# Kernel optimization log

Measured on AMD Instinct MI355X. Metric: run time of the kernel, lower is better.

The kernel has to match this reference:

```python
import jax, jax.numpy as jnp
import numpy as np
import math

KERNEL_SIZES = [3, 5, 7, 7, 9, 9]
DILATIONS = [1, 2, 1, 3, 1, 2]
NUM_HEADS = 6
HEAD_DIM = 32  # in_channels 192 / 6 heads


def _neighborhood_patches(t, k, dil):
    """Equivalent of F.unfold(t, kernel_size=k, dilation=dil, padding=dil*(k//2)).
    t: [B, d, H, W] -> [B, d, k*k, H, W] (zero-padded borders, torch unfold ordering:
    patch index p = i*k + j over the kernel window, row-major)."""
    B, d, H, W = t.shape
    pad = dil * (k // 2)
    tp = jnp.pad(t, ((0, 0), (0, 0), (pad, pad), (pad, pad)))
    pats = [tp[:, :, i * dil:i * dil + H, j * dil:j * dil + W]
            for i in range(k) for j in range(k)]
    return jnp.stack(pats, axis=2)


def setup_inputs() -> dict:
    key = jax.random.key(0)
    ks = jax.random.split(key, 3 + NUM_HEADS)
    B, C, H, W = 4, 192, 96, 96
    x = jax.random.normal(ks[0], (B, C, H, W), dtype=jnp.float32)
    w_qkv = jax.random.normal(ks[1], (3 * C, C), dtype=jnp.float32) * 0.02  # 1x1 conv weight
    w_out = jax.random.normal(ks[2], (C, C), dtype=jnp.float32) * 0.02      # 1x1 conv weight
    inp = {"x": x, "w_qkv": w_qkv, "w_out": w_out}
    for i, k in enumerate(KERNEL_SIZES):
        # module inits biases to zeros; use small randn so softmax path is exercised
        inp[f"b{i}"] = jax.random.normal(ks[3 + i], (k * k,), dtype=jnp.float32) * 0.02
    return inp


def reference(x, w_qkv, w_out, b0, b1, b2, b3, b4, b5):
    biases = [b0, b1, b2, b3, b4, b5]
    B, C, H, W = x.shape
    scale = 1.0 / math.sqrt(HEAD_DIM)
    # 1x1 conv qkv projection
    qkv = jnp.einsum('bchw,oc->bohw', x, w_qkv)
    q, k, v = jnp.split(qkv, 3, axis=1)
    q = q.reshape(B, NUM_HEADS, HEAD_DIM, H, W)
    k = k.reshape(B, NUM_HEADS, HEAD_DIM, H, W)
    v = v.reshape(B, NUM_HEADS, HEAD_DIM, H, W)
    head_outs = []
    for i in range(NUM_HEADS):  # heads have structurally different (k, dilation)
        ksz, dil = KERNEL_SIZES[i], DILATIONS[i]
        kp = _neighborhood_patches(k[:, i], ksz, dil)  # [B, d, k*k, H, W]
        vp = _neighborhood_patches(v[:, i], ksz, dil)  # [B, d, k*k, H, W]
        scores = jnp.einsum('bdhw,bdphw->bphw', q[:, i], kp) * scale
        scores = scores + biases[i][None, :, None, None]
        attn = jax.nn.softmax(scores, axis=1)  # softmax over the k*k neighborhood
        head_outs.append(jnp.einsum('bphw,bdphw->bdhw', attn, vp))
    out = jnp.concatenate(head_outs, axis=1)  # [B, C, H, W]
    return jnp.einsum('bchw,oc->bohw', out, w_out)
```

## Files before the change

kernel.cpp:

```cpp
#include <hip/hip_runtime.h>
#include <hip/hip_bf16.h>
#include <math.h>

#define NPIX 9216
#define HDIM 96
#define WDIM 96
#define NHEADS 6
#define BATCH 4

typedef __bf16 bf16x8 __attribute__((ext_vector_type(8)));
typedef float  f32x4  __attribute__((ext_vector_type(4)));

struct Bias6 { const float* p[6]; };

__device__ __forceinline__ void cp16(void* ldst, const void* gsrc) {
    __builtin_amdgcn_global_load_lds(
        (const __attribute__((address_space(1))) unsigned int*)gsrc,
        (__attribute__((address_space(3))) unsigned int*)ldst, 16, 0, 0);
}

__device__ __forceinline__ unsigned short bfbits(__bf16 x) { return *(unsigned short*)&x; }

__device__ __forceinline__ unsigned packf16(float a, float b) {
    _Float16 ha = (_Float16)a, hb = (_Float16)b;
    return (unsigned)*(unsigned short*)&ha | ((unsigned)*(unsigned short*)&hb << 16);
}

template<int N>
__device__ __forceinline__ void waitcnt_vm() {
    if constexpr (N == 0) asm volatile("s_waitcnt vmcnt(0)" ::: "memory");
    else if constexpr (N == 2) asm volatile("s_waitcnt vmcnt(2)" ::: "memory");
    else if constexpr (N == 3) asm volatile("s_waitcnt vmcnt(3)" ::: "memory");
    else if constexpr (N == 5) asm volatile("s_waitcnt vmcnt(5)" ::: "memory");
    else asm volatile("s_waitcnt vmcnt(0)" ::: "memory");
    __builtin_amdgcn_sched_barrier(0);
}

#define MIX_LL(acc, kk, qq) asm("v_fma_mix_f32 %0, %1, %2, %0 op_sel:[0,0,0] op_sel_hi:[1,1,0]" : "+v"(acc) : "v"(kk), "v"(qq))
#define MIX_HH(acc, kk, qq) asm("v_fma_mix_f32 %0, %1, %2, %0 op_sel:[1,1,0] op_sel_hi:[1,1,0]" : "+v"(acc) : "v"(kk), "v"(qq))
#define MIX_LF(acc, vv, ee) asm("v_fma_mix_f32 %0, %1, %2, %0 op_sel:[0,0,0] op_sel_hi:[1,0,0]" : "+v"(acc) : "v"(vv), "v"(ee))
#define MIX_HF(acc, vv, ee) asm("v_fma_mix_f32 %0, %1, %2, %0 op_sel:[1,0,0] op_sel_hi:[1,0,0]" : "+v"(acc) : "v"(vv), "v"(ee))

__global__ __launch_bounds__(256) void convert_w(
    const float* __restrict__ w1, __bf16* __restrict__ h1, __bf16* __restrict__ l1, int n1,
    const float* __restrict__ w2, __bf16* __restrict__ h2, __bf16* __restrict__ l2, int n2)
{
    const int i = blockIdx.x * 256 + threadIdx.x;
    if (i < n1) { float f = w1[i]; __bf16 h = (__bf16)f; h1[i] = h; l1[i] = (__bf16)(f - (float)h); }
    if (i < n2) { float f = w2[i]; __bf16 h = (__bf16)f; h2[i] = h; l2[i] = (__bf16)(f - (float)h); }
}

__global__ __launch_bounds__(256) void convert_x(
    const float* __restrict__ x, __bf16* __restrict__ Xh)
{
    __shared__ float t[32][65];
    const int b  = blockIdx.z;
    const int c0 = blockIdx.y * 32;
    const int p0 = blockIdx.x * 64;
    const int tid = threadIdx.x;
    const int pl = tid & 63;
    #pragma unroll
    for (int i = 0; i < 8; ++i) {
        const int c = i * 4 + (tid >> 6);
        t[c][pl] = x[((size_t)b * 192 + c0 + c) * NPIX + p0 + pl];
    }
    __syncthreads();
    const int p  = tid >> 2;
    const int cq = (tid & 3) * 8;
    bf16x8 vh;
    #pragma unroll
    for (int j = 0; j < 8; ++j)
        vh[j] = (__bf16)t[cq + j][p];
    *(bf16x8*)(Xh + ((size_t)b * NPIX + p0 + p) * 192 + c0 + cq) = vh;
}

template<int MODE>
__global__ __launch_bounds__(256) void gemm_mfma(
    const __bf16* __restrict__ Ah, const __bf16* __restrict__ Al,
    const __bf16* __restrict__ Bh,
    void* __restrict__ Yv, int M)
{
    __shared__ __bf16 sAh[64 * 64];
    __shared__ __bf16 sAl[64 * 64];
    __shared__ __bf16 sBh[128 * 64];

    const int b  = blockIdx.z;
    const int n0 = blockIdx.x * 128;
    const int m0 = blockIdx.y * 64;
    const int tid  = threadIdx.x;
    const int lane = tid & 63;
    const int wid  = tid >> 6;
    const int wr = wid >> 1, wc = wid & 1;
    const int lr = lane & 15;
    const int kg = lane >> 4;

    const char* gA_h = (const char*)Ah + (size_t)m0 * 384;
    const char* gA_l = (const char*)Al + (size_t)m0 * 384;
    const char* gB   = (const char*)Bh + ((size_t)b * NPIX + n0) * 384;

    f32x4 acc[2][4];
    #pragma unroll
    for (int mf = 0; mf < 2; ++mf)
        #pragma unroll
        for (int nf = 0; nf < 4; ++nf)
            acc[mf][nf] = (f32x4){0.f, 0.f, 0.f, 0.f};

    for (int ks = 0; ks < 3; ++ks) {
        if (ks) __syncthreads();
        const int kb = ks * 128;
        #pragma unroll
        for (int it = 0; it < 2; ++it) {
            const int d  = it * 256 + tid;
            const int rd = d >> 3, cd = d & 7;
            const size_t src = (size_t)rd * 384 + kb + ((cd ^ (rd & 7)) << 4);
            cp16((char*)sAh + d * 16, gA_h + src);
            cp16((char*)sAl + d * 16, gA_l + src);
        }
        #pragma unroll
        for (int it = 0; it < 4; ++it) {
            const int d  = it * 256 + tid;
            const int rd = d >> 3, cd = d & 7;
            const size_t src = (size_t)rd * 384 + kb + ((cd ^ (rd & 7)) << 4);
            cp16((char*)sBh + d * 16, gB + src);
        }
        __syncthreads();
        #pragma unroll
        for (int s = 0; s < 2; ++s) {
            bf16x8 aH[2], aL[2], bH[4];
            #pragma unroll
            for (int mf = 0; mf < 2; ++mf) {
                const int row = wr * 32 + mf * 16 + lr;
                const int c = (s * 4 + kg) ^ (row & 7);
                aH[mf] = *(const bf16x8*)((const char*)sAh + row * 128 + c * 16);
                aL[mf] = *(const bf16x8*)((const char*)sAl + row * 128 + c * 16);
            }
            #pragma unroll
            for (int nf = 0; nf < 4; ++nf) {
                const int row = wc * 64 + nf * 16 + lr;
                const int c = (s * 4 + kg) ^ (row & 7);
                bH[nf] = *(const bf16x8*)((const char*)sBh + row * 128 + c * 16);
            }
            #pragma unroll
            for (int mf = 0; mf < 2; ++mf)
                #pragma unroll
                for (int nf = 0; nf < 4; ++nf) {
                    acc[mf][nf] = __builtin_amdgcn_mfma_f32_16x16x32_bf16(aH[mf], bH[nf], acc[mf][nf], 0, 0, 0);
                    acc[mf][nf] = __builtin_amdgcn_mfma_f32_16x16x32_bf16(aL[mf], bH[nf], acc[mf][nf], 0, 0, 0);
                }
        }
    }

    if (MODE == 0) {
        float* Yb = (float*)Yv + ((size_t)b * M + m0 + wr * 32) * NPIX + n0 + wc * 64;
        #pragma unroll
        for (int mf = 0; mf < 2; ++mf)
            #pragma unroll
            for (int r = 0; r < 4; ++r) {
                const int row = mf * 16 + kg * 4 + r;
                #pragma unroll
                for (int nf = 0; nf < 4; ++nf)
                    Yb[(size_t)row * NPIX + nf * 16 + lr] = acc[mf][nf][r];
            }
    } else {
        #pragma unroll
        for (int mf = 0; mf < 2; ++mf) {
            const int cbase = m0 + wr * 32 + mf * 16 + kg * 4;
            unsigned* Yq = (unsigned*)Yv
                + (((size_t)b * 72 + (cbase >> 3)) * NPIX + n0 + wc * 64 + lr) * 4
                + ((kg & 1) << 1);
            #pragma unroll
            for (int nf = 0; nf < 4; ++nf) {
                Yq[(nf * 16) * 4 + 0] = packf16(acc[mf][nf][0], acc[mf][nf][1]);
                Yq[(nf * 16) * 4 + 1] = packf16(acc[mf][nf][2], acc[mf][nf][3]);
            }
        }
    }
}

template<int KSZ, int DIL, bool DB, int L>
__device__ __forceinline__ void attn_body(
    const uint4* __restrict__ Qq, const uint4* __restrict__ Kq,
    const uint4* __restrict__ Vq, const float* __restrict__ bias,
    const uint4* __restrict__ guard,
    __bf16* __restrict__ oh, int h0, int w0,
    uint4* __restrict__ bufs,
    unsigned (* __restrict__ out_lds)[256])
{
    constexpr int CC  = KSZ / 2;
    constexpr int HAL = CC * DIL;
    constexpr int R   = 8 + 2 * HAL;
    constexpr int C   = 32 + 2 * HAL;
    constexpr int RC  = R * C;
    constexpr int NN  = KSZ * KSZ;
    const float scale = 0.17677669529663689f;

    const int tid = threadIdx.x;
    const int tx = tid & 31;
    const int ty = tid >> 5;
    const int pix = (h0 + ty) * WDIM + (w0 + tx);
    const int lb = ty * C + tx;

    uint4 qv[4];
    #pragma unroll
    for (int p = 0; p < 4; ++p) qv[p] = Qq[(size_t)p * NPIX + pix];

    float score[NN];
    #pragma unroll
    for (int n = 0; n < NN; ++n) score[n] = bias[n] * 5.656854249492381f;

    auto STAGE = [&](int r) {
        const uint4* src = (r < 4) ? (Kq + (size_t)r * NPIX)
                                   : (Vq + (size_t)(r - 4) * NPIX);
        uint4* dst = bufs + (DB ? ((r & 1) * (L * 256)) : 0);
        #pragma unroll
        for (int it = 0; it < L; ++it) {
            const int idx = it * 256 + tid;
            const int rr = idx / C, cc = idx - rr * C;
            const int gh = h0 - HAL + rr, gw = w0 - HAL + cc;
            const bool ok = (idx < RC) && ((unsigned)gh < (unsigned)HDIM)
                                       && ((unsigned)gw < (unsigned)WDIM);
            const uint4* s = ok ? (src + gh * WDIM + gw) : guard;
            cp16(dst + idx, s);
        }
    };

    auto QK = [&](const uint4* buf, int oct) {
        const uint4 q = qv[oct];
        #pragma unroll
        for (int i = 0; i < KSZ; ++i)
            #pragma unroll
            for (int j = 0; j < KSZ; ++j) {
                const uint4 k8 = buf[lb + i * DIL * C + j * DIL];
                float s = score[i * KSZ + j];
                MIX_LL(s, k8.x, q.x); MIX_HH(s, k8.x, q.x);
                MIX_LL(s, k8.y, q.y); MIX_HH(s, k8.y, q.y);
                MIX_LL(s, k8.z, q.z); MIX_HH(s, k8.z, q.z);
                MIX_LL(s, k8.w, q.w); MIX_HH(s, k8.w, q.w);
                score[i * KSZ + j] = s;
            }
    };

    float inv = 0.f;
    auto SOFTMAX = [&]() {
        float l = 0.f;
        #pragma unroll
        for (int n = 0; n < NN; ++n) {
            const float e = __expf(score[n] * scale);
            l += e;
            score[n] = e;
        }
        inv = 1.f / l;
    };

    auto PV = [&](const uint4* buf, int oct) {
        float a0 = 0.f, a1 = 0.f, a2 = 0.f, a3 = 0.f;
        float a4 = 0.f, a5 = 0.f, a6 = 0.f, a7 = 0.f;
        #pragma unroll
        for (int i = 0; i < KSZ; ++i)
            #pragma unroll
            for (int j = 0; j < KSZ; ++j) {
                const uint4 v8 = buf[lb + i * DIL * C + j * DIL];
                const float e = score[i * KSZ + j];
                MIX_LF(a0, v8.x, e); MIX_HF(a1, v8.x, e);
                MIX_LF(a2, v8.y, e); MIX_HF(a3, v8.y, e);
                MIX_LF(a4, v8.z, e); MIX_HF(a5, v8.z, e);
                MIX_LF(a6, v8.w, e); MIX_HF(a7, v8.w, e);
            }
        const int rr = oct & 1;
        const __bf16 c0 = (__bf16)(a0 * inv), c1 = (__bf16)(a1 * inv);
        const __bf16 c2 = (__bf16)(a2 * inv), c3 = (__bf16)(a3 * inv);
        const __bf16 c4 = (__bf16)(a4 * inv), c5 = (__bf16)(a5 * inv);
        const __bf16 c6 = (__bf16)(a6 * inv), c7 = (__bf16)(a7 * inv);
        out_lds[rr * 4 + 0][tid] = (unsigned)bfbits(c0) | ((unsigned)bfbits(c1) << 16);
        out_lds[rr * 4 + 1][tid] = (unsigned)bfbits(c2) | ((unsigned)bfbits(c3) << 16);
        out_lds[rr * 4 + 2][tid] = (unsigned)bfbits(c4) | ((unsigned)bfbits(c5) << 16);
        out_lds[rr * 4 + 3][tid] = (unsigned)bfbits(c6) | ((unsigned)bfbits(c7) << 16);
    };

    auto COOP = [&](int half) {
        #pragma unroll
        for (int it = 0; it < 2; ++it) {
            const int linear = it * 256 + tid;
            const int px = linear >> 1;
            const int c  = linear & 1;
            const int gpix = (h0 + (px >> 5)) * WDIM + w0 + (px & 31);
            uint4 val = make_uint4(out_lds[c * 4 + 0][px], out_lds[c * 4 + 1][px],
                                   out_lds[c * 4 + 2][px], out_lds[c * 4 + 3][px]);
            *((uint4*)((unsigned*)(oh + (size_t)gpix * 192)) + half * 2 + c) = val;
        }
    };

    if constexpr (DB) {
        STAGE(0);
        #pragma unroll
        for (int r = 0; r < 8; ++r) {
            if (r < 7) STAGE(r + 1);
            if (r < 7) waitcnt_vm<L>(); else waitcnt_vm<0>();
            __builtin_amdgcn_s_barrier();
            __builtin_amdgcn_sched_barrier(0);
            const uint4* buf = bufs + (r & 1) * (L * 256);
            if (r < 4) {
                QK(buf, r);
                if (r == 3) SOFTMAX();
            } else {
                PV(buf, r - 4);
                asm volatile("s_waitcnt lgkmcnt(0)" ::: "memory");
                __builtin_amdgcn_sched_barrier(0);
            }
            __builtin_amdgcn_s_barrier();
            __builtin_amdgcn_sched_barrier(0);
            if (r == 5) COOP(0);
            if (r == 7) COOP(1);
        }
    } else {
        #pragma unroll
        for (int r = 0; r < 8; ++r) {
            __syncthreads();
            if (r == 6) COOP(0);
            STAGE(r);
            __syncthreads();
            const uint4* buf = bufs;
            if (r < 4) {
                QK(buf, r);
                if (r == 3) SOFTMAX();
            } else {
                PV(buf, r - 4);
            }
        }
        __syncthreads();
        COOP(1);
    }
}

__global__ __launch_bounds__(256) void attn_kernel(
    const uint4* __restrict__ qkv, Bias6 bs, __bf16* __restrict__ ATh,
    const uint4* __restrict__ guard)
{
    __shared__ uint4 bufs[2560];
    __shared__ unsigned out_lds[8][256];

    const int orig = blockIdx.x;
    const int wg = (orig & 7) * 108 + (orig >> 3);
    const int panel = wg / 36;
    const int tile = wg - panel * 36;
    const int chunk = panel / 3, slot = panel - chunk * 3;
    int head, b;
    if (slot == 0)      { head = 4 + (chunk >> 2); b = chunk & 3; }
    else if (slot == 1) { head = 2 + (chunk >> 2); b = chunk & 3; }
    else                { head = (chunk < 4) ? 1 : 0; b = chunk & 3; }
    const int tx = tile % 3, ty = tile / 3;
    const int w0 = tx * 32, h0 = ty * 8;

    const uint4* base = qkv + (size_t)b * 72 * NPIX;
    const uint4* Qq = base + (size_t)(head * 4) * NPIX;
    const uint4* Kq = base + (size_t)(24 + head * 4) * NPIX;
    const uint4* Vq = base + (size_t)(48 + head * 4) * NPIX;
    __bf16* oh = ATh + (size_t)b * NPIX * 192 + head * 32;
    const float* bias = bs.p[head];

    switch (head) {
        case 0: attn_body<3, 1, true, 2>(Qq, Kq, Vq, bias, guard, oh, h0, w0, bufs, out_lds); break;
        case 1: attn_body<5, 2, true, 3>(Qq, Kq, Vq, bias, guard, oh, h0, w0, bufs, out_lds); break;
        case 2: attn_body<7, 1, true, 3>(Qq, Kq, Vq, bias, guard, oh, h0, w0, bufs, out_lds); break;
        case 3: attn_body<7, 3, false, 6>(Qq, Kq, Vq, bias, guard, oh, h0, w0, bufs, out_lds); break;
        case 4: attn_body<9, 1, true, 3>(Qq, Kq, Vq, bias, guard, oh, h0, w0, bufs, out_lds); break;
        case 5: attn_body<9, 2, true, 5>(Qq, Kq, Vq, bias, guard, oh, h0, w0, bufs, out_lds); break;
    }
}

extern "C" void kernel_launch(void* const* d_in, const int* in_sizes, int n_in,
                              void* d_out, int out_size, void* d_ws, size_t ws_size,
                              hipStream_t stream) {
    const float* x     = (const float*)d_in[0];
    const float* w_qkv = (const float*)d_in[1];
    const float* w_out = (const float*)d_in[2];
    Bias6 bs;
    for (int i = 0; i < 6; ++i) bs.p[i] = (const float*)d_in[3 + i];
    float* out = (float*)d_out;

    char* ws = (char*)d_ws;
    uint4* QKV = (uint4*)ws;            ws += (size_t)BATCH * 72 * NPIX * 16;
    __bf16* Xh  = (__bf16*)ws;          ws += (size_t)BATCH * NPIX * 192 * 2;
    __bf16* ATh = (__bf16*)ws;          ws += (size_t)BATCH * NPIX * 192 * 2;
    __bf16* W1h = (__bf16*)ws;          ws += (size_t)576 * 192 * 2;
    __bf16* W1l = (__bf16*)ws;          ws += (size_t)576 * 192 * 2;
    __bf16* W2h = (__bf16*)ws;          ws += (size_t)192 * 192 * 2;
    __bf16* W2l = (__bf16*)ws;          ws += (size_t)192 * 192 * 2;
    uint4* guard = (uint4*)ws;          ws += 1024;

    hipMemsetAsync(guard, 0, 1024, stream);

    convert_w<<<dim3((576 * 192 + 255) / 256), 256, 0, stream>>>(
        w_qkv, W1h, W1l, 576 * 192, w_out, W2h, W2l, 192 * 192);
    convert_x<<<dim3(NPIX / 64, 192 / 32, BATCH), 256, 0, stream>>>(x, Xh);

    gemm_mfma<1><<<dim3(NPIX / 128, 576 / 64, BATCH), 256, 0, stream>>>(
        W1h, W1l, Xh, (void*)QKV, 576);

    attn_kernel<<<dim3(864), 256, 0, stream>>>(QKV, bs, ATh, guard);

    gemm_mfma<0><<<dim3(NPIX / 128, 192 / 64, BATCH), 256, 0, stream>>>(
        W2h, W2l, ATh, (void*)out, 192);
}
```

Before: 94.70 us.

## Drop low-bf16 weight correction for Q/K and output GEMMs, fuse weight conversion

Merges the weight split-conversion into the x conversion kernel to remove a launch. The QKV GEMM now applies the low-part bf16 correction MFMA only for V rows, and the output projection GEMM skips it entirely, halving MFMA and LDS traffic there. Softmax uses exp2f with a pre-folded log2e*scale constant. This trades some numerical accuracy in the Q/K scores and final output for less compute.

```diff
diff --git a/kernel.cpp b/kernel.cpp
--- a/kernel.cpp
+++ b/kernel.cpp
@@ -41,23 +41,33 @@
 #define MIX_LF(acc, vv, ee) asm("v_fma_mix_f32 %0, %1, %2, %0 op_sel:[0,0,0] op_sel_hi:[1,0,0]" : "+v"(acc) : "v"(vv), "v"(ee))
 #define MIX_HF(acc, vv, ee) asm("v_fma_mix_f32 %0, %1, %2, %0 op_sel:[1,0,0] op_sel_hi:[1,0,0]" : "+v"(acc) : "v"(vv), "v"(ee))
 
-__global__ __launch_bounds__(256) void convert_w(
-    const float* __restrict__ w1, __bf16* __restrict__ h1, __bf16* __restrict__ l1, int n1,
-    const float* __restrict__ w2, __bf16* __restrict__ h2, __bf16* __restrict__ l2, int n2)
-{
-    const int i = blockIdx.x * 256 + threadIdx.x;
-    if (i < n1) { float f = w1[i]; __bf16 h = (__bf16)f; h1[i] = h; l1[i] = (__bf16)(f - (float)h); }
-    if (i < n2) { float f = w2[i]; __bf16 h = (__bf16)f; h2[i] = h; l2[i] = (__bf16)(f - (float)h); }
-}
-
 __global__ __launch_bounds__(256) void convert_x(
-    const float* __restrict__ x, __bf16* __restrict__ Xh)
+    const float* __restrict__ x, __bf16* __restrict__ Xh,
+    const float* __restrict__ w1, __bf16* __restrict__ h1, __bf16* __restrict__ l1,
+    const float* __restrict__ w2, __bf16* __restrict__ h2, __bf16* __restrict__ l2)
 {
     __shared__ float t[32][65];
     const int b  = blockIdx.z;
     const int c0 = blockIdx.y * 32;
     const int p0 = blockIdx.x * 64;
     const int tid = threadIdx.x;
+
+    if (blockIdx.y == 0 && blockIdx.z == 0) {
+        const int f = blockIdx.x * 256 + tid;
+        #pragma unroll
+        for (int u = 0; u < 4; ++u) {
+            const int i = f * 4 + u;
+            if (i < 576 * 192) {
+                float v = w1[i]; __bf16 h = (__bf16)v;
+                h1[i] = h; l1[i] = (__bf16)(v - (float)h);
+            } else {
+                const int j = i - 576 * 192;
+                float v = w2[j]; __bf16 h = (__bf16)v;
+                h2[j] = h; l2[j] = (__bf16)(v - (float)h);
+            }
+        }
+    }
+
     const int pl = tid & 63;
     #pragma unroll
     for (int i = 0; i < 8; ++i) {
@@ -74,7 +84,7 @@
     *(bf16x8*)(Xh + ((size_t)b * NPIX + p0 + p) * 192 + c0 + cq) = vh;
 }
 
-template<int MODE>
+template<int MODE, int TWO_FROM>
 __global__ __launch_bounds__(256) void gemm_mfma(
     const __bf16* __restrict__ Ah, const __bf16* __restrict__ Al,
     const __bf16* __restrict__ Bh,
@@ -87,6 +97,7 @@
     const int b  = blockIdx.z;
     const int n0 = blockIdx.x * 128;
     const int m0 = blockIdx.y * 64;
+    const bool two = (TWO_FROM < 1024) && (m0 >= TWO_FROM);
     const int tid  = threadIdx.x;
     const int lane = tid & 63;
     const int wid  = tid >> 6;
@@ -114,7 +125,7 @@
             const int rd = d >> 3, cd = d & 7;
             const size_t src = (size_t)rd * 384 + kb + ((cd ^ (rd & 7)) << 4);
             cp16((char*)sAh + d * 16, gA_h + src);
-            cp16((char*)sAl + d * 16, gA_l + src);
+            if (two) cp16((char*)sAl + d * 16, gA_l + src);
         }
         #pragma unroll
         for (int it = 0; it < 4; ++it) {
@@ -132,7 +143,7 @@
                 const int row = wr * 32 + mf * 16 + lr;
                 const int c = (s * 4 + kg) ^ (row & 7);
                 aH[mf] = *(const bf16x8*)((const char*)sAh + row * 128 + c * 16);
-                aL[mf] = *(const bf16x8*)((const char*)sAl + row * 128 + c * 16);
+                if (two) aL[mf] = *(const bf16x8*)((const char*)sAl + row * 128 + c * 16);
             }
             #pragma unroll
             for (int nf = 0; nf < 4; ++nf) {
@@ -145,7 +156,8 @@
                 #pragma unroll
                 for (int nf = 0; nf < 4; ++nf) {
                     acc[mf][nf] = __builtin_amdgcn_mfma_f32_16x16x32_bf16(aH[mf], bH[nf], acc[mf][nf], 0, 0, 0);
-                    acc[mf][nf] = __builtin_amdgcn_mfma_f32_16x16x32_bf16(aL[mf], bH[nf], acc[mf][nf], 0, 0, 0);
+                    if (two)
+                        acc[mf][nf] = __builtin_amdgcn_mfma_f32_16x16x32_bf16(aL[mf], bH[nf], acc[mf][nf], 0, 0, 0);
                 }
         }
     }
@@ -192,7 +204,6 @@
     constexpr int C   = 32 + 2 * HAL;
     constexpr int RC  = R * C;
     constexpr int NN  = KSZ * KSZ;
-    const float scale = 0.17677669529663689f;
 
     const int tid = threadIdx.x;
     const int tx = tid & 31;
@@ -245,7 +256,7 @@
         float l = 0.f;
         #pragma unroll
         for (int n = 0; n < NN; ++n) {
-            const float e = __expf(score[n] * scale);
+            const float e = exp2f(score[n] * 0.25506113952980654f);
             l += e;
             score[n] = e;
         }
@@ -390,15 +401,14 @@
 
     hipMemsetAsync(guard, 0, 1024, stream);
 
-    convert_w<<<dim3((576 * 192 + 255) / 256), 256, 0, stream>>>(
-        w_qkv, W1h, W1l, 576 * 192, w_out, W2h, W2l, 192 * 192);
-    convert_x<<<dim3(NPIX / 64, 192 / 32, BATCH), 256, 0, stream>>>(x, Xh);
-
-    gemm_mfma<1><<<dim3(NPIX / 128, 576 / 64, BATCH), 256, 0, stream>>>(
+    convert_x<<<dim3(NPIX / 64, 192 / 32, BATCH), 256, 0, stream>>>(
+        x, Xh, w_qkv, W1h, W1l, w_out, W2h, W2l);
+
+    gemm_mfma<1, 384><<<dim3(NPIX / 128, 576 / 64, BATCH), 256, 0, stream>>>(
         W1h, W1l, Xh, (void*)QKV, 576);
 
     attn_kernel<<<dim3(864), 256, 0, stream>>>(QKV, bs, ATh, guard);
 
-    gemm_mfma<0><<<dim3(NPIX / 128, 192 / 64, BATCH), 256, 0, stream>>>(
+    gemm_mfma<0, 1024><<<dim3(NPIX / 128, 192 / 64, BATCH), 256, 0, stream>>>(
         W2h, W2l, ATh, (void*)out, 192);
 }
```

After: 91.35 us. 3.5% less time.
